# Performance work log

Hardware: AMD Instinct MI355X
Metric: run time of the kernel (lower is better)

The kernel has to match this reference:

```python
import jax, jax.numpy as jnp
import numpy as np

N = 50000
E = 800000
D_IN = 256
HID = 256
EPS = 1e-12


def _glorot(key, shape):
    fan_in, fan_out = shape[1], shape[0]
    lim = jnp.sqrt(6.0 / (fan_in + fan_out))
    return jax.random.uniform(key, shape, jnp.float32, -lim, lim)


def setup_inputs() -> dict:
    key = jax.random.key(0)
    ks = jax.random.split(key, 8)
    x = jax.random.normal(ks[0], (N, D_IN), jnp.float32)
    edge_index = jax.random.randint(ks[1], (2, E), 0, N, jnp.int64)
    # SAGEConv params: lin_l (neighbor, with bias), lin_r (root, no bias)
    W1l = _glorot(ks[2], (HID, D_IN))
    b1l = jnp.zeros((HID,), jnp.float32)
    W1r = _glorot(ks[3], (HID, D_IN))
    W2l = _glorot(ks[4], (HID, HID))
    b2l = jnp.zeros((HID,), jnp.float32)
    W2r = _glorot(ks[5], (HID, HID))
    return {"x": x, "edge_index": edge_index,
            "W1l": W1l, "b1l": b1l, "W1r": W1r,
            "W2l": W2l, "b2l": b2l, "W2r": W2r}


def _sage_conv(x, src, dst, Wl, bl, Wr, num_nodes):
    # mean aggregation of source features onto destination nodes
    agg = jax.ops.segment_sum(x[src], dst, num_segments=num_nodes)          # [N, d]
    cnt = jax.ops.segment_sum(jnp.ones((src.shape[0],), x.dtype), dst,
                              num_segments=num_nodes)                        # [N]
    mean = agg / jnp.maximum(cnt, 1.0)[:, None]
    out = mean @ Wl.T + bl + x @ Wr.T                                        # [N, out]
    # L2 normalize (normalize=True)
    norm = jnp.linalg.norm(out, axis=-1, keepdims=True)
    return out / jnp.maximum(norm, EPS)


def reference(x, edge_index, W1l, b1l, W1r, W2l, b2l, W2r):
    src, dst = edge_index[0], edge_index[1]
    n = x.shape[0]
    h = _sage_conv(x, src, dst, W1l, b1l, W1r, n)
    h = jax.nn.relu(h)
    h = _sage_conv(h, src, dst, W2l, b2l, W2r, n)
    return h
```

## Files before the change

kernel.cpp:

```cpp
#include <hip/hip_runtime.h>
#include <hip/hip_bf16.h>


#define DD 256
#define NPB 128

typedef unsigned short ushort_t;
using bf16x8 = __attribute__((ext_vector_type(8))) short;
using f32x4  = __attribute__((ext_vector_type(4))) float;

static __device__ __forceinline__ float b2f(ushort_t u) {
    __hip_bfloat16 h = *reinterpret_cast<__hip_bfloat16*>(&u);
    return __bfloat162float(h);
}
static __device__ __forceinline__ ushort_t f2b(float f) {
    __hip_bfloat16 h = __float2bfloat16(f);
    return *reinterpret_cast<ushort_t*>(&h);
}

static __device__ __forceinline__ void load16(const ushort_t* g, ushort_t* l) {
    __builtin_amdgcn_global_load_lds(
        (const __attribute__((address_space(1))) unsigned*)(g),
        (__attribute__((address_space(3))) unsigned*)(l),
        16, 0, 0);
}


__global__ __launch_bounds__(256) void prep_kernel(
        const int* __restrict__ ei, int* __restrict__ cnt, int E, int eb,
        const float* __restrict__ x, ushort_t* __restrict__ abuf, int xe, int cxb,
        const float* __restrict__ w1l, const float* __restrict__ w1r,
        const float* __restrict__ w2l, const float* __restrict__ w2r,
        ushort_t* __restrict__ wc1, ushort_t* __restrict__ wc2) {
    int b = blockIdx.x;
    if (b < eb) {
        int e = b * 256 + threadIdx.x;
        if (e < E) atomicAdd(&cnt[ei[E + e]], 1);
        return;
    }
    b -= eb;
    if (b < cxb) {
        int i = (b * 256 + threadIdx.x) * 8;
        if (i + 8 > xe) return;
        int row = i >> 8, col = i & 255;
        float4 a = *(const float4*)(x + i);
        float4 c = *(const float4*)(x + i + 4);
        ushort_t o[8] = {f2b(a.x), f2b(a.y), f2b(a.z), f2b(a.w),
                         f2b(c.x), f2b(c.y), f2b(c.z), f2b(c.w)};
        *(int4*)(abuf + (size_t)row * 512 + 256 + col) = *(const int4*)o;
        return;
    }
    b -= cxb;
    {
        int i = (b * 256 + threadIdx.x) * 8;
        int which = i >> 16;
        int o = i & 65535;
        int row = o >> 8, col = o & 255;
        const float* src = (which == 0) ? w1l : (which == 1) ? w1r
                          : (which == 2) ? w2l : w2r;
        ushort_t* dst = ((which < 2) ? wc1 : wc2)
                        + (size_t)row * 512 + (which & 1) * 256 + col;
        float4 a = *(const float4*)(src + o);
        float4 c = *(const float4*)(src + o + 4);
        ushort_t ov[8] = {f2b(a.x), f2b(a.y), f2b(a.z), f2b(a.w),
                          f2b(c.x), f2b(c.y), f2b(c.z), f2b(c.w)};
        *(int4*)dst = *(const int4*)ov;
    }
}


__global__ __launch_bounds__(256) void scan_partial_kernel(const int* __restrict__ cnt,
                                                           int* __restrict__ part, int n) {
    __shared__ int ws[4];
    int tid = threadIdx.x;
    int wave = tid >> 6, lane = tid & 63;
    int i0 = blockIdx.x * 2048 + tid * 8;
    int sum = 0;
    if (i0 + 8 <= n) {
        int4 a = *(const int4*)(cnt + i0);
        int4 b = *(const int4*)(cnt + i0 + 4);
        sum = a.x + a.y + a.z + a.w + b.x + b.y + b.z + b.w;
    } else {
        for (int j = i0; j < n; j++) sum += cnt[j];
    }
    #pragma unroll
    for (int off = 1; off < 64; off <<= 1) sum += __shfl_xor(sum, off);
    if (lane == 0) ws[wave] = sum;
    __syncthreads();
    if (tid == 0) part[blockIdx.x] = ws[0] + ws[1] + ws[2] + ws[3];
}

__global__ __launch_bounds__(256) void scan_final_kernel(const int* __restrict__ cnt,
                                                         const int* __restrict__ part,
                                                         int* __restrict__ offs,
                                                         int* __restrict__ bcur,
                                                         int n, int E, int nb) {
    __shared__ int wt[4];
    __shared__ int sbase;
    int tid = threadIdx.x;
    int wave = tid >> 6, lane = tid & 63;
    if (tid < 64) {
        int pv = (tid < nb) ? part[tid] : 0;
        int incl = pv;
        #pragma unroll
        for (int off = 1; off < 64; off <<= 1) {
            int t = __shfl_up(incl, off);
            if (tid >= off) incl += t;
        }
        if (tid == (int)blockIdx.x) sbase = incl - pv;
    }
    int i0 = blockIdx.x * 2048 + tid * 8;
    int v[8], s[8];
    int run = 0;
    if (i0 + 8 <= n) {
        int4 a = *(const int4*)(cnt + i0);
        int4 b = *(const int4*)(cnt + i0 + 4);
        v[0] = a.x; v[1] = a.y; v[2] = a.z; v[3] = a.w;
        v[4] = b.x; v[5] = b.y; v[6] = b.z; v[7] = b.w;
    } else {
        #pragma unroll
        for (int j = 0; j < 8; j++) v[j] = (i0 + j < n) ? cnt[i0 + j] : 0;
    }
    #pragma unroll
    for (int j = 0; j < 8; j++) { run += v[j]; s[j] = run; }
    int tsum = run;
    int incl = tsum;
    #pragma unroll
    for (int off = 1; off < 64; off <<= 1) {
        int t = __shfl_up(incl, off);
        if (lane >= off) incl += t;
    }
    if (lane == 63) wt[wave] = incl;
    __syncthreads();
    int woff = 0;
    for (int w = 0; w < wave; w++) woff += wt[w];
    int texcl = sbase + woff + (incl - tsum);
    #pragma unroll
    for (int j = 0; j < 8; j++) {
        int idx = i0 + j;
        if (idx < n) {
            int e = texcl + s[j] - v[j];
            offs[idx] = e;
            if ((idx & (NPB - 1)) == 0) bcur[idx / NPB] = e;
        }
    }
    if (blockIdx.x == 0 && tid == 0) offs[n] = E;
}


__global__ __launch_bounds__(256) void part_kernel(const int* __restrict__ ei,
                                                   int* __restrict__ bcur,
                                                   int2* __restrict__ stage,
                                                   int E, int nbuck) {
    __shared__ int hist[512];
    __shared__ int gbase[512];
    int tid = threadIdx.x;
    for (int i = tid; i < nbuck; i += 256) hist[i] = 0;
    __syncthreads();
    int sv[8], dv[8], bk[8], rk[8];
    #pragma unroll
    for (int j = 0; j < 8; j++) {
        int e = blockIdx.x * 2048 + j * 256 + tid;
        if (e < E) {
            sv[j] = ei[e];
            dv[j] = ei[E + e];
            bk[j] = dv[j] / NPB;
            rk[j] = atomicAdd(&hist[bk[j]], 1);
        } else bk[j] = -1;
    }
    __syncthreads();
    for (int i = tid; i < nbuck; i += 256) {
        int h = hist[i];
        gbase[i] = h ? atomicAdd(&bcur[i], h) : 0;
    }
    __syncthreads();
    #pragma unroll
    for (int j = 0; j < 8; j++)
        if (bk[j] >= 0) {
            int p = gbase[bk[j]] + rk[j];
            stage[p] = make_int2(sv[j], dv[j]);
        }
}

__global__ __launch_bounds__(256) void group_kernel(const int2* __restrict__ stage,
                                                    const int* __restrict__ offs,
                                                    int* __restrict__ csr, int N) {
    __shared__ int lcur[NPB];
    int b = blockIdx.x;
    int lo = b * NPB;
    int hi = min(N, lo + NPB);
    int tid = threadIdx.x;
    if (tid < hi - lo) lcur[tid] = offs[lo + tid];
    __syncthreads();
    int base = offs[lo];
    int m = offs[hi] - base;
    for (int t = tid; t < m; t += 256) {
        int2 v = stage[base + t];
        int p = atomicAdd(&lcur[v.y - lo], 1);
        csr[p] = v.x;
    }
}


static __device__ __forceinline__ void add8(float* acc, int4 v) {
    const unsigned* u = (const unsigned*)&v;
    #pragma unroll
    for (int j = 0; j < 4; j++) {
        acc[2 * j]     += __uint_as_float(u[j] << 16);
        acc[2 * j + 1] += __uint_as_float(u[j] & 0xffff0000u);
    }
}

__global__ __launch_bounds__(256) void agg_kernel(const ushort_t* __restrict__ X,
                                                  const int* __restrict__ csr,
                                                  const int* __restrict__ offs,
                                                  ushort_t* __restrict__ mean, int N) {
    int wv = threadIdx.x >> 6;
    int lane = threadIdx.x & 63;
    int half = lane >> 5;
    int c = lane & 31;
    int node = blockIdx.x * 4 + wv;
    if (node >= N) return;
    int beg = offs[node], end = offs[node + 1];

    float acc[8];
    #pragma unroll
    for (int j = 0; j < 8; j++) acc[j] = 0.f;

    const ushort_t* base = X + (size_t)c * 8;
    int i = beg;
    for (; i + 8 <= end; i += 8) {
        int s0 = csr[i + half];
        int s1 = csr[i + 2 + half];
        int s2 = csr[i + 4 + half];
        int s3 = csr[i + 6 + half];
        int4 v0 = *(const int4*)(base + (size_t)s0 * 512);
        int4 v1 = *(const int4*)(base + (size_t)s1 * 512);
        int4 v2 = *(const int4*)(base + (size_t)s2 * 512);
        int4 v3 = *(const int4*)(base + (size_t)s3 * 512);
        add8(acc, v0); add8(acc, v1); add8(acc, v2); add8(acc, v3);
    }
    for (; i + 2 <= end; i += 2) {
        int s0 = csr[i + half];
        int4 v0 = *(const int4*)(base + (size_t)s0 * 512);
        add8(acc, v0);
    }
    if (i < end && half == 0) {
        int s0 = csr[i];
        int4 v0 = *(const int4*)(base + (size_t)s0 * 512);
        add8(acc, v0);
    }

    #pragma unroll
    for (int j = 0; j < 8; j++) acc[j] += __shfl_xor(acc[j], 32);

    if (half == 0) {
        float scale = 1.f / fmaxf((float)(end - beg), 1.f);
        ushort_t o[8];
        #pragma unroll
        for (int j = 0; j < 8; j++) o[j] = f2b(acc[j] * scale);
        *(int4*)(mean + (size_t)node * 512 + c * 8) = *(const int4*)o;
    }
}


__global__ __launch_bounds__(512, 4) void gemm_norm_kernel(
        const ushort_t* __restrict__ abuf,
        const ushort_t* __restrict__ W,
        const float*    __restrict__ bias,
        ushort_t* __restrict__ outb,
        float*    __restrict__ outf,
        int ostride,
        int N, int relu) {
    __shared__ union {
        struct {
            ushort_t As[128 * 64];
            ushort_t Bs[256 * 64];
        } s;
        ushort_t ebuf[64 * 264];
    } u;
    __shared__ float rowsq[128];

    int tid = threadIdx.x;
    int wave = tid >> 6, lane = tid & 63;
    int quad = lane >> 4, m16 = lane & 15;
    int swz = m16 & 7;
    int rowhalf = wave >> 2;
    int colq = wave & 3;
    int rowbase = blockIdx.x * 128;

    if (tid < 128) rowsq[tid] = 0.f;

    f32x4 acc[4][4];
    #pragma unroll
    for (int i = 0; i < 4; i++)
        #pragma unroll
        for (int j = 0; j < 4; j++)
            acc[i][j] = (f32x4){0.f, 0.f, 0.f, 0.f};

    const ushort_t* Ag = abuf + (size_t)rowbase * 512;

    for (int ki = 0; ki < 8; ki++) {
        int kb = ki * 64;
        __syncthreads();
        #pragma unroll
        for (int t = 0; t < 2; t++) {
            int instr = wave * 2 + t;
            int flat = instr * 64 + lane;
            int row = flat >> 3, cc = flat & 7;
            int ccg = cc ^ (row & 7);
            load16(Ag + (size_t)row * 512 + kb + ccg * 8, &u.s.As[instr * 512]);
        }
        #pragma unroll
        for (int t = 0; t < 4; t++) {
            int instr = wave * 4 + t;
            int flat = instr * 64 + lane;
            int row = flat >> 3, cc = flat & 7;
            int ccg = cc ^ (row & 7);
            load16(W + (size_t)row * 512 + kb + ccg * 8, &u.s.Bs[instr * 512]);
        }
        __syncthreads();

        #pragma unroll
        for (int ks = 0; ks < 2; ks++) {
            int cbase = ks * 4 + quad;
            bf16x8 af[4], bfr[4];
            #pragma unroll
            for (int rt = 0; rt < 4; rt++) {
                int r = rowhalf * 64 + rt * 16 + m16;
                af[rt] = *(const bf16x8*)&u.s.As[r * 64 + (cbase ^ swz) * 8];
            }
            #pragma unroll
            for (int ct = 0; ct < 4; ct++) {
                int r = colq * 64 + ct * 16 + m16;
                bfr[ct] = *(const bf16x8*)&u.s.Bs[r * 64 + (cbase ^ swz) * 8];
            }
            #pragma unroll
            for (int rt = 0; rt < 4; rt++)
                #pragma unroll
                for (int ct = 0; ct < 4; ct++)
                    acc[rt][ct] = __builtin_amdgcn_mfma_f32_16x16x32_bf16(
                        af[rt], bfr[ct], acc[rt][ct], 0, 0, 0);
        }
    }

    float bvals[4];
    #pragma unroll
    for (int ct = 0; ct < 4; ct++)
        bvals[ct] = bias[colq * 64 + ct * 16 + m16];
    #pragma unroll
    for (int rt = 0; rt < 4; rt++) {
        #pragma unroll
        for (int reg = 0; reg < 4; reg++) {
            float s = 0.f;
            #pragma unroll
            for (int ct = 0; ct < 4; ct++) {
                float v = acc[rt][ct][reg] + bvals[ct];
                acc[rt][ct][reg] = v;
                s += v * v;
            }
            #pragma unroll
            for (int off = 1; off < 16; off <<= 1)
                s += __shfl_xor(s, off);
            if (m16 == 0)
                atomicAdd(&rowsq[rowhalf * 64 + rt * 16 + quad * 4 + reg], s);
        }
    }
    __syncthreads();

    #pragma unroll
    for (int p = 0; p < 2; p++) {
        if (rowhalf == p) {
            #pragma unroll
            for (int rt = 0; rt < 4; rt++) {
                #pragma unroll
                for (int reg = 0; reg < 4; reg++) {
                    int rl = rt * 16 + quad * 4 + reg;
                    float inv = 1.f / fmaxf(sqrtf(rowsq[p * 64 + rl]), 1e-12f);
                    #pragma unroll
                    for (int ct = 0; ct < 4; ct++) {
                        float v = acc[rt][ct][reg] * inv;
                        if (relu) v = fmaxf(v, 0.f);
                        int col = colq * 64 + ct * 16 + m16;
                        u.ebuf[rl * 264 + col] = f2b(v);
                    }
                }
            }
        }
        __syncthreads();
        #pragma unroll
        for (int j = 0; j < 4; j++) {
            int flat = j * 512 + tid;
            int row = flat >> 5, cc = flat & 31;
            int gr = rowbase + p * 64 + row;
            if (gr < N) {
                bf16x8 v = *(const bf16x8*)&u.ebuf[row * 264 + cc * 8];
                if (outf) {
                    float4 f0, f1;
                    f0.x = b2f((ushort_t)v[0]); f0.y = b2f((ushort_t)v[1]);
                    f0.z = b2f((ushort_t)v[2]); f0.w = b2f((ushort_t)v[3]);
                    f1.x = b2f((ushort_t)v[4]); f1.y = b2f((ushort_t)v[5]);
                    f1.z = b2f((ushort_t)v[6]); f1.w = b2f((ushort_t)v[7]);
                    float* ptr = outf + (size_t)gr * ostride + cc * 8;
                    *(float4*)ptr = f0;
                    *(float4*)(ptr + 4) = f1;
                } else {
                    *(bf16x8*)(outb + (size_t)gr * ostride + cc * 8) = v;
                }
            }
        }
        __syncthreads();
    }
}


static inline size_t align_up(size_t x, size_t a) { return (x + a - 1) & ~(a - 1); }

extern "C" void kernel_launch(void* const* d_in, const int* in_sizes, int n_in,
                              void* d_out, int out_size, void* d_ws, size_t ws_size,
                              hipStream_t stream) {
    const float* x   = (const float*)d_in[0];
    const int*   ei  = (const int*)d_in[1];
    const float* W1l = (const float*)d_in[2];
    const float* b1l = (const float*)d_in[3];
    const float* W1r = (const float*)d_in[4];
    const float* W2l = (const float*)d_in[5];
    const float* b2l = (const float*)d_in[6];
    const float* W2r = (const float*)d_in[7];

    int N = in_sizes[0] / DD;
    int E = in_sizes[1] / 2;
    int nbuck = (N + NPB - 1) / NPB;

    char* ws = (char*)d_ws;
    size_t off = 0;
    int* cnt = (int*)(ws + off);      off = align_up(off + (size_t)N * 4, 256);
    int* offs = (int*)(ws + off);     off = align_up(off + (size_t)(N + 1) * 4, 256);
    int* bcur = (int*)(ws + off);     off = align_up(off + (size_t)512 * 4, 256);
    int* part = (int*)(ws + off);     off = align_up(off + (size_t)64 * 4, 256);
    int* csr = (int*)(ws + off);      off = align_up(off + (size_t)E * 4, 256);
    int2* stage = (int2*)(ws + off);  off = align_up(off + (size_t)E * 8, 256);
    ushort_t* abuf = (ushort_t*)(ws + off);  off = align_up(off + (size_t)N * 512 * 2, 256);
    ushort_t* wc1 = (ushort_t*)(ws + off);   off = align_up(off + (size_t)256 * 512 * 2, 256);
    ushort_t* wc2 = (ushort_t*)(ws + off);   off = align_up(off + (size_t)256 * 512 * 2, 256);

    hipMemsetAsync(cnt, 0, (size_t)N * 4, stream);

    int xe = N * DD;
    int eb = (E + 255) / 256;
    int cxb = (xe / 8 + 255) / 256;
    int cwb = (4 * DD * DD / 8) / 256;
    prep_kernel<<<eb + cxb + cwb, 256, 0, stream>>>(ei, cnt, E, eb,
                                                    x, abuf, xe, cxb,
                                                    W1l, W1r, W2l, W2r, wc1, wc2);

    int nb = (N + 2047) / 2048;
    scan_partial_kernel<<<nb, 256, 0, stream>>>(cnt, part, N);
    scan_final_kernel<<<nb, 256, 0, stream>>>(cnt, part, offs, bcur, N, E, nb);

    int pb = (E + 2047) / 2048;
    part_kernel<<<pb, 256, 0, stream>>>(ei, bcur, stage, E, nbuck);
    group_kernel<<<nbuck, 256, 0, stream>>>(stage, offs, csr, N);

    int gb = (N + 127) / 128;
    int ab = (N + 3) / 4;

    agg_kernel<<<ab, 256, 0, stream>>>(abuf + 256, csr, offs, abuf, N);
    gemm_norm_kernel<<<gb, 512, 0, stream>>>(abuf, wc1, b1l,
                                             abuf + 256, (float*)nullptr, 512, N, 1);

    agg_kernel<<<ab, 256, 0, stream>>>(abuf + 256, csr, offs, abuf, N);
    gemm_norm_kernel<<<gb, 512, 0, stream>>>(abuf, wc2, b2l,
                                             (ushort_t*)nullptr, (float*)d_out, DD, N, 0);
}
```

Before: 331.3 us.

## Fuse neighbor mean aggregation into the SAGE GEMM+normalize kernel

Merges the separate aggregation kernel into the GEMM kernel. Each block of 64 rows first gathers and averages neighbor features directly into swizzled shared memory, then uses them as the first K half of the GEMM. This removes the global round-trip of the mean buffer and two launches. The interleaved [mean|x] buffer is replaced by separate compact x and h buffers with 256-element row stride. Tiles shrink to 64 rows with 256 threads, so each block covers fewer rows and must reload the full weight tile for each. The gather phase runs serially per wave before any MMA work, with no overlap.

```diff
diff --git a/kernel.cpp b/kernel.cpp
--- a/kernel.cpp
+++ b/kernel.cpp
@@ -28,7 +28,7 @@
 
 __global__ __launch_bounds__(256) void prep_kernel(
         const int* __restrict__ ei, int* __restrict__ cnt, int E, int eb,
-        const float* __restrict__ x, ushort_t* __restrict__ abuf, int xe, int cxb,
+        const float* __restrict__ x, ushort_t* __restrict__ xb, int xe, int cxb,
         const float* __restrict__ w1l, const float* __restrict__ w1r,
         const float* __restrict__ w2l, const float* __restrict__ w2r,
         ushort_t* __restrict__ wc1, ushort_t* __restrict__ wc2) {
@@ -42,12 +42,11 @@
     if (b < cxb) {
         int i = (b * 256 + threadIdx.x) * 8;
         if (i + 8 > xe) return;
-        int row = i >> 8, col = i & 255;
         float4 a = *(const float4*)(x + i);
         float4 c = *(const float4*)(x + i + 4);
         ushort_t o[8] = {f2b(a.x), f2b(a.y), f2b(a.z), f2b(a.w),
                          f2b(c.x), f2b(c.y), f2b(c.z), f2b(c.w)};
-        *(int4*)(abuf + (size_t)row * 512 + 256 + col) = *(const int4*)o;
+        *(int4*)(xb + i) = *(const int4*)o;
         return;
     }
     b -= cxb;
@@ -202,94 +201,112 @@
 }
 
 
-static __device__ __forceinline__ void add8(float* acc, int4 v) {
-    const unsigned* u = (const unsigned*)&v;
-    #pragma unroll
-    for (int j = 0; j < 4; j++) {
-        acc[2 * j]     += __uint_as_float(u[j] << 16);
-        acc[2 * j + 1] += __uint_as_float(u[j] & 0xffff0000u);
-    }
-}
-
-__global__ __launch_bounds__(256) void agg_kernel(const ushort_t* __restrict__ X,
-                                                  const int* __restrict__ csr,
-                                                  const int* __restrict__ offs,
-                                                  ushort_t* __restrict__ mean, int N) {
-    int wv = threadIdx.x >> 6;
-    int lane = threadIdx.x & 63;
-    int half = lane >> 5;
-    int c = lane & 31;
-    int node = blockIdx.x * 4 + wv;
-    if (node >= N) return;
-    int beg = offs[node], end = offs[node + 1];
-
-    float acc[8];
-    #pragma unroll
-    for (int j = 0; j < 8; j++) acc[j] = 0.f;
-
-    const ushort_t* base = X + (size_t)c * 8;
-    int i = beg;
-    for (; i + 8 <= end; i += 8) {
-        int s0 = csr[i + half];
-        int s1 = csr[i + 2 + half];
-        int s2 = csr[i + 4 + half];
-        int s3 = csr[i + 6 + half];
-        int4 v0 = *(const int4*)(base + (size_t)s0 * 512);
-        int4 v1 = *(const int4*)(base + (size_t)s1 * 512);
-        int4 v2 = *(const int4*)(base + (size_t)s2 * 512);
-        int4 v3 = *(const int4*)(base + (size_t)s3 * 512);
-        add8(acc, v0); add8(acc, v1); add8(acc, v2); add8(acc, v3);
-    }
-    for (; i + 2 <= end; i += 2) {
-        int s0 = csr[i + half];
-        int4 v0 = *(const int4*)(base + (size_t)s0 * 512);
-        add8(acc, v0);
-    }
-    if (i < end && half == 0) {
-        int s0 = csr[i];
-        int4 v0 = *(const int4*)(base + (size_t)s0 * 512);
-        add8(acc, v0);
-    }
-
-    #pragma unroll
-    for (int j = 0; j < 8; j++) acc[j] += __shfl_xor(acc[j], 32);
-
-    if (half == 0) {
-        float scale = 1.f / fmaxf((float)(end - beg), 1.f);
-        ushort_t o[8];
-        #pragma unroll
-        for (int j = 0; j < 8; j++) o[j] = f2b(acc[j] * scale);
-        *(int4*)(mean + (size_t)node * 512 + c * 8) = *(const int4*)o;
-    }
-}
-
-
-__global__ __launch_bounds__(512, 4) void gemm_norm_kernel(
-        const ushort_t* __restrict__ abuf,
+__global__ __launch_bounds__(256, 2) void sage_layer_kernel(
+        const ushort_t* __restrict__ xsrc,
+        const int* __restrict__ csr,
+        const int* __restrict__ offs,
         const ushort_t* __restrict__ W,
         const float*    __restrict__ bias,
         ushort_t* __restrict__ outb,
         float*    __restrict__ outf,
-        int ostride,
         int N, int relu) {
     __shared__ union {
         struct {
-            ushort_t As[128 * 64];
+            ushort_t Ms[4 * 4096];
+            ushort_t As[64 * 64];
             ushort_t Bs[256 * 64];
         } s;
         ushort_t ebuf[64 * 264];
     } u;
-    __shared__ float rowsq[128];
+    __shared__ float rowsq[64];
 
     int tid = threadIdx.x;
     int wave = tid >> 6, lane = tid & 63;
     int quad = lane >> 4, m16 = lane & 15;
     int swz = m16 & 7;
-    int rowhalf = wave >> 2;
-    int colq = wave & 3;
-    int rowbase = blockIdx.x * 128;
-
-    if (tid < 128) rowsq[tid] = 0.f;
+    int rowbase = blockIdx.x * 64;
+
+    if (tid < 64) rowsq[tid] = 0.f;
+
+    {
+        int half = lane >> 5;
+        int c = lane & 31;
+        const ushort_t* base = xsrc + (size_t)c * 8;
+        for (int j = 0; j < 16; j++) {
+            int r = wave * 16 + j;
+            int node = rowbase + r;
+            if (node >= N) break;
+            int beg = offs[node], end = offs[node + 1];
+            float acc[8];
+            #pragma unroll
+            for (int q = 0; q < 8; q++) acc[q] = 0.f;
+            int i = beg;
+            for (; i + 8 <= end; i += 8) {
+                int s0 = csr[i + half];
+                int s1 = csr[i + 2 + half];
+                int s2 = csr[i + 4 + half];
+                int s3 = csr[i + 6 + half];
+                int4 v0 = *(const int4*)(base + (size_t)s0 * 256);
+                int4 v1 = *(const int4*)(base + (size_t)s1 * 256);
+                int4 v2 = *(const int4*)(base + (size_t)s2 * 256);
+                int4 v3 = *(const int4*)(base + (size_t)s3 * 256);
+                {   const unsigned* uu = (const unsigned*)&v0;
+                    #pragma unroll
+                    for (int q = 0; q < 4; q++) {
+                        acc[2*q]   += __uint_as_float(uu[q] << 16);
+                        acc[2*q+1] += __uint_as_float(uu[q] & 0xffff0000u);
+                    } }
+                {   const unsigned* uu = (const unsigned*)&v1;
+                    #pragma unroll
+                    for (int q = 0; q < 4; q++) {
+                        acc[2*q]   += __uint_as_float(uu[q] << 16);
+                        acc[2*q+1] += __uint_as_float(uu[q] & 0xffff0000u);
+                    } }
+                {   const unsigned* uu = (const unsigned*)&v2;
+                    #pragma unroll
+                    for (int q = 0; q < 4; q++) {
+                        acc[2*q]   += __uint_as_float(uu[q] << 16);
+                        acc[2*q+1] += __uint_as_float(uu[q] & 0xffff0000u);
+                    } }
+                {   const unsigned* uu = (const unsigned*)&v3;
+                    #pragma unroll
+                    for (int q = 0; q < 4; q++) {
+                        acc[2*q]   += __uint_as_float(uu[q] << 16);
+                        acc[2*q+1] += __uint_as_float(uu[q] & 0xffff0000u);
+                    } }
+            }
+            for (; i + 2 <= end; i += 2) {
+                int s0 = csr[i + half];
+                int4 v0 = *(const int4*)(base + (size_t)s0 * 256);
+                const unsigned* uu = (const unsigned*)&v0;
+                #pragma unroll
+                for (int q = 0; q < 4; q++) {
+                    acc[2*q]   += __uint_as_float(uu[q] << 16);
+                    acc[2*q+1] += __uint_as_float(uu[q] & 0xffff0000u);
+                }
+            }
+            if (i < end && half == 0) {
+                int s0 = csr[i];
+                int4 v0 = *(const int4*)(base + (size_t)s0 * 256);
+                const unsigned* uu = (const unsigned*)&v0;
+                #pragma unroll
+                for (int q = 0; q < 4; q++) {
+                    acc[2*q]   += __uint_as_float(uu[q] << 16);
+                    acc[2*q+1] += __uint_as_float(uu[q] & 0xffff0000u);
+                }
+            }
+            #pragma unroll
+            for (int q = 0; q < 8; q++) acc[q] += __shfl_xor(acc[q], 32);
+            if (half == 0) {
+                float scale = 1.f / fmaxf((float)(end - beg), 1.f);
+                ushort_t o[8];
+                #pragma unroll
+                for (int q = 0; q < 8; q++) o[q] = f2b(acc[q] * scale);
+                *(bf16x8*)&u.s.Ms[(c >> 3) * 4096 + r * 64 + ((c & 7) ^ (r & 7)) * 8] =
+                    *(const bf16x8*)o;
+            }
+        }
+    }
 
     f32x4 acc[4][4];
     #pragma unroll
@@ -298,41 +315,47 @@
         for (int j = 0; j < 4; j++)
             acc[i][j] = (f32x4){0.f, 0.f, 0.f, 0.f};
 
-    const ushort_t* Ag = abuf + (size_t)rowbase * 512;
+    const ushort_t* Ag = xsrc + (size_t)rowbase * 256;
 
     for (int ki = 0; ki < 8; ki++) {
-        int kb = ki * 64;
         __syncthreads();
-        #pragma unroll
-        for (int t = 0; t < 2; t++) {
-            int instr = wave * 2 + t;
-            int flat = instr * 64 + lane;
-            int row = flat >> 3, cc = flat & 7;
-            int ccg = cc ^ (row & 7);
-            load16(Ag + (size_t)row * 512 + kb + ccg * 8, &u.s.As[instr * 512]);
-        }
-        #pragma unroll
-        for (int t = 0; t < 4; t++) {
-            int instr = wave * 4 + t;
-            int flat = instr * 64 + lane;
-            int row = flat >> 3, cc = flat & 7;
-            int ccg = cc ^ (row & 7);
-            load16(W + (size_t)row * 512 + kb + ccg * 8, &u.s.Bs[instr * 512]);
+        if (ki >= 4) {
+            int kb = (ki - 4) * 64;
+            #pragma unroll
+            for (int t = 0; t < 2; t++) {
+                int instr = wave * 2 + t;
+                int flat = instr * 64 + lane;
+                int row = flat >> 3, cc = flat & 7;
+                int ccg = cc ^ (row & 7);
+                load16(Ag + (size_t)row * 256 + kb + ccg * 8, &u.s.As[instr * 512]);
+            }
+        }
+        {
+            int kb = ki * 64;
+            #pragma unroll
+            for (int t = 0; t < 8; t++) {
+                int instr = wave * 8 + t;
+                int flat = instr * 64 + lane;
+                int row = flat >> 3, cc = flat & 7;
+                int ccg = cc ^ (row & 7);
+                load16(W + (size_t)row * 512 + kb + ccg * 8, &u.s.Bs[instr * 512]);
+            }
         }
         __syncthreads();
 
+        const ushort_t* Abase = (ki < 4) ? &u.s.Ms[ki * 4096] : u.s.As;
         #pragma unroll
         for (int ks = 0; ks < 2; ks++) {
             int cbase = ks * 4 + quad;
             bf16x8 af[4], bfr[4];
             #pragma unroll
             for (int rt = 0; rt < 4; rt++) {
-                int r = rowhalf * 64 + rt * 16 + m16;
-                af[rt] = *(const bf16x8*)&u.s.As[r * 64 + (cbase ^ swz) * 8];
+                int r = rt * 16 + m16;
+                af[rt] = *(const bf16x8*)&Abase[r * 64 + (cbase ^ swz) * 8];
             }
             #pragma unroll
             for (int ct = 0; ct < 4; ct++) {
-                int r = colq * 64 + ct * 16 + m16;
+                int r = wave * 64 + ct * 16 + m16;
                 bfr[ct] = *(const bf16x8*)&u.s.Bs[r * 64 + (cbase ^ swz) * 8];
             }
             #pragma unroll
@@ -347,7 +370,7 @@
     float bvals[4];
     #pragma unroll
     for (int ct = 0; ct < 4; ct++)
-        bvals[ct] = bias[colq * 64 + ct * 16 + m16];
+        bvals[ct] = bias[wave * 64 + ct * 16 + m16];
     #pragma unroll
     for (int rt = 0; rt < 4; rt++) {
         #pragma unroll
@@ -363,53 +386,48 @@
             for (int off = 1; off < 16; off <<= 1)
                 s += __shfl_xor(s, off);
             if (m16 == 0)
-                atomicAdd(&rowsq[rowhalf * 64 + rt * 16 + quad * 4 + reg], s);
-        }
-    }
-    __syncthreads();
-
-    #pragma unroll
-    for (int p = 0; p < 2; p++) {
-        if (rowhalf == p) {
-            #pragma unroll
-            for (int rt = 0; rt < 4; rt++) {
-                #pragma unroll
-                for (int reg = 0; reg < 4; reg++) {
-                    int rl = rt * 16 + quad * 4 + reg;
-                    float inv = 1.f / fmaxf(sqrtf(rowsq[p * 64 + rl]), 1e-12f);
-                    #pragma unroll
-                    for (int ct = 0; ct < 4; ct++) {
-                        float v = acc[rt][ct][reg] * inv;
-                        if (relu) v = fmaxf(v, 0.f);
-                        int col = colq * 64 + ct * 16 + m16;
-                        u.ebuf[rl * 264 + col] = f2b(v);
-                    }
-                }
-            }
-        }
-        __syncthreads();
-        #pragma unroll
-        for (int j = 0; j < 4; j++) {
-            int flat = j * 512 + tid;
-            int row = flat >> 5, cc = flat & 31;
-            int gr = rowbase + p * 64 + row;
-            if (gr < N) {
-                bf16x8 v = *(const bf16x8*)&u.ebuf[row * 264 + cc * 8];
-                if (outf) {
-                    float4 f0, f1;
-                    f0.x = b2f((ushort_t)v[0]); f0.y = b2f((ushort_t)v[1]);
-                    f0.z = b2f((ushort_t)v[2]); f0.w = b2f((ushort_t)v[3]);
-                    f1.x = b2f((ushort_t)v[4]); f1.y = b2f((ushort_t)v[5]);
-                    f1.z = b2f((ushort_t)v[6]); f1.w = b2f((ushort_t)v[7]);
-                    float* ptr = outf + (size_t)gr * ostride + cc * 8;
-                    *(float4*)ptr = f0;
-                    *(float4*)(ptr + 4) = f1;
-                } else {
-                    *(bf16x8*)(outb + (size_t)gr * ostride + cc * 8) = v;
-                }
-            }
-        }
-        __syncthreads();
+                atomicAdd(&rowsq[rt * 16 + quad * 4 + reg], s);
+        }
+    }
+    __syncthreads();
+
+    #pragma unroll
+    for (int rt = 0; rt < 4; rt++) {
+        #pragma unroll
+        for (int reg = 0; reg < 4; reg++) {
+            int rl = rt * 16 + quad * 4 + reg;
+            float inv = 1.f / fmaxf(sqrtf(rowsq[rl]), 1e-12f);
+            #pragma unroll
+            for (int ct = 0; ct < 4; ct++) {
+                float v = acc[rt][ct][reg] * inv;
+                if (relu) v = fmaxf(v, 0.f);
+                int col = wave * 64 + ct * 16 + m16;
+                u.ebuf[rl * 264 + col] = f2b(v);
+            }
+        }
+    }
+    __syncthreads();
+
+    #pragma unroll
+    for (int j = 0; j < 8; j++) {
+        int flat = j * 256 + tid;
+        int row = flat >> 5, cc = flat & 31;
+        int gr = rowbase + row;
+        if (gr < N) {
+            bf16x8 v = *(const bf16x8*)&u.ebuf[row * 264 + cc * 8];
+            if (outf) {
+                float4 f0, f1;
+                f0.x = b2f((ushort_t)v[0]); f0.y = b2f((ushort_t)v[1]);
+                f0.z = b2f((ushort_t)v[2]); f0.w = b2f((ushort_t)v[3]);
+                f1.x = b2f((ushort_t)v[4]); f1.y = b2f((ushort_t)v[5]);
+                f1.z = b2f((ushort_t)v[6]); f1.w = b2f((ushort_t)v[7]);
+                float* ptr = outf + (size_t)gr * 256 + cc * 8;
+                *(float4*)ptr = f0;
+                *(float4*)(ptr + 4) = f1;
+            } else {
+                *(bf16x8*)(outb + (size_t)gr * 256 + cc * 8) = v;
+            }
+        }
     }
 }
 
@@ -440,7 +458,8 @@
     int* part = (int*)(ws + off);     off = align_up(off + (size_t)64 * 4, 256);
     int* csr = (int*)(ws + off);      off = align_up(off + (size_t)E * 4, 256);
     int2* stage = (int2*)(ws + off);  off = align_up(off + (size_t)E * 8, 256);
-    ushort_t* abuf = (ushort_t*)(ws + off);  off = align_up(off + (size_t)N * 512 * 2, 256);
+    ushort_t* xb = (ushort_t*)(ws + off);  off = align_up(off + (size_t)N * 256 * 2, 256);
+    ushort_t* hb = (ushort_t*)(ws + off);  off = align_up(off + (size_t)N * 256 * 2, 256);
     ushort_t* wc1 = (ushort_t*)(ws + off);   off = align_up(off + (size_t)256 * 512 * 2, 256);
     ushort_t* wc2 = (ushort_t*)(ws + off);   off = align_up(off + (size_t)256 * 512 * 2, 256);
 
@@ -451,7 +470,7 @@
     int cxb = (xe / 8 + 255) / 256;
     int cwb = (4 * DD * DD / 8) / 256;
     prep_kernel<<<eb + cxb + cwb, 256, 0, stream>>>(ei, cnt, E, eb,
-                                                    x, abuf, xe, cxb,
+                                                    x, xb, xe, cxb,
                                                     W1l, W1r, W2l, W2r, wc1, wc2);
 
     int nb = (N + 2047) / 2048;
@@ -462,14 +481,10 @@
     part_kernel<<<pb, 256, 0, stream>>>(ei, bcur, stage, E, nbuck);
     group_kernel<<<nbuck, 256, 0, stream>>>(stage, offs, csr, N);
 
-    int gb = (N + 127) / 128;
-    int ab = (N + 3) / 4;
-
-    agg_kernel<<<ab, 256, 0, stream>>>(abuf + 256, csr, offs, abuf, N);
-    gemm_norm_kernel<<<gb, 512, 0, stream>>>(abuf, wc1, b1l,
-                                             abuf + 256, (float*)nullptr, 512, N, 1);
-
-    agg_kernel<<<ab, 256, 0, stream>>>(abuf + 256, csr, offs, abuf, N);
-    gemm_norm_kernel<<<gb, 512, 0, stream>>>(abuf, wc2, b2l,
-                                             (ushort_t*)nullptr, (float*)d_out, DD, N, 0);
-}
+    int gb = (N + 63) / 64;
+
+    sage_layer_kernel<<<gb, 256, 0, stream>>>(xb, csr, offs, wc1, b1l,
+                                              hb, (float*)nullptr, N, 1);
+    sage_layer_kernel<<<gb, 256, 0, stream>>>(hb, csr, offs, wc2, b2l,
+                                              (ushort_t*)nullptr, (float*)d_out, N, 0);
+}
```

New measurement: 431.8 us. 1.3x slower.
